# Optimization experiments

Hardware: AMD Instinct MI355X
Metric: run time of the kernel (lower is better)

Reference implementation:

```python
import jax, jax.numpy as jnp
import numpy as np

WH, WW = 12, 12
N_TOK = WH * WW          # 144
DIM = 512
HEADS = 16
NW = 64                  # windows per image
B_ = 256                 # num_windows * batch
CPB_HIDDEN = 512


def _rel_tables():
    # continuous relative coords table (SwinV2 cpb input), shape (1, 2Wh-1, 2Ww-1, 2)
    ch = np.arange(-(WH - 1), WH, dtype=np.float32)
    cw = np.arange(-(WW - 1), WW, dtype=np.float32)
    gh, gw = np.meshgrid(ch, cw, indexing='ij')
    table = np.stack([gh, gw], axis=-1)[None]
    table[..., 0] /= (WH - 1)
    table[..., 1] /= (WW - 1)
    table *= 8.0
    table = np.sign(table) * np.log2(np.abs(table) + 1.0) / np.log2(8.0)
    # relative position index, shape (N, N), values in [0, (2Wh-1)*(2Ww-1))
    coords = np.stack(np.meshgrid(np.arange(WH), np.arange(WW), indexing='ij'))
    cf = coords.reshape(2, -1)
    rel = (cf[:, :, None] - cf[:, None, :]).transpose(1, 2, 0).astype(np.int64)
    rel[..., 0] += WH - 1
    rel[..., 1] += WW - 1
    rel[..., 0] *= 2 * WW - 1
    idx = rel.sum(-1)
    return table.astype(np.float32), idx


def setup_inputs() -> dict:
    key = jax.random.key(0)
    ks = jax.random.split(key, 10)
    table, idx = _rel_tables()
    x = jax.random.normal(ks[0], (B_, N_TOK, DIM), dtype=jnp.float32)
    # 0 / -100 additive mask (shifted-window style), shape (nW, N, N)
    mask = jnp.where(jax.random.uniform(ks[1], (NW, N_TOK, N_TOK)) < 0.9, 0.0, -100.0).astype(jnp.float32)
    s = 0.02
    return {
        'x': x,
        'mask': mask,
        'qkv_w': s * jax.random.normal(ks[2], (3 * DIM, DIM), dtype=jnp.float32),
        'qkv_b': jnp.zeros((3 * DIM,), dtype=jnp.float32),
        'proj_w': s * jax.random.normal(ks[3], (DIM, DIM), dtype=jnp.float32),
        'proj_b': jnp.zeros((DIM,), dtype=jnp.float32),
        'cpb_w1': s * jax.random.normal(ks[4], (CPB_HIDDEN, 2), dtype=jnp.float32),
        'cpb_b1': jnp.zeros((CPB_HIDDEN,), dtype=jnp.float32),
        'cpb_w2': s * jax.random.normal(ks[5], (HEADS, CPB_HIDDEN), dtype=jnp.float32),
        'rel_table': jnp.asarray(table),
        'rel_index': jnp.asarray(idx, dtype=jnp.int32),
    }


def reference(x, mask, qkv_w, qkv_b, proj_w, proj_b, cpb_w1, cpb_b1, cpb_w2, rel_table, rel_index):
    Bw, N, C = x.shape
    H = cpb_w2.shape[0]
    hd = C // H
    scale = hd ** -0.5
    qkv = (x @ qkv_w.T + qkv_b).reshape(Bw, N, 3, H, hd).transpose(2, 0, 3, 1, 4)
    q, k, v = qkv[0], qkv[1], qkv[2]          # each (Bw, H, N, hd)
    attn = jnp.einsum('bhnd,bhmd->bhnm', q * scale, k)
    # continuous relative position bias: MLP on coord table then gather
    tbl = jax.nn.relu(rel_table @ cpb_w1.T + cpb_b1) @ cpb_w2.T   # (1, 2Wh-1, 2Ww-1, H)
    tbl = tbl.reshape(-1, H)
    bias = tbl[rel_index.reshape(-1)].reshape(N, N, H).transpose(2, 0, 1)  # (H, N, N)
    attn = attn + bias[None]
    nW = mask.shape[0]
    attn = attn.reshape(Bw // nW, nW, H, N, N) + mask[None, :, None]
    attn = jax.nn.softmax(attn.reshape(Bw, H, N, N), axis=-1)
    out = jnp.einsum('bhnm,bhmd->bhnd', attn, v).transpose(0, 2, 1, 3).reshape(Bw, N, C)
    return out @ proj_w.T + proj_b
```

## Files before the change

kernel.cpp:

```cpp
#include <hip/hip_runtime.h>


using f32x4  = __attribute__((ext_vector_type(4))) float;
using bf16x8 = __attribute__((ext_vector_type(8))) short;

__device__ __forceinline__ unsigned short f2bf(float f) {
  unsigned u = __float_as_uint(f);
  u = (u + 0x7fffu + ((u >> 16) & 1u)) >> 16;
  return (unsigned short)u;
}
__device__ __forceinline__ float bf2f(unsigned short s) {
  return __uint_as_float(((unsigned)s) << 16);
}

typedef __attribute__((address_space(1))) unsigned int as1_u32;
typedef __attribute__((address_space(3))) unsigned int as3_u32;

__device__ __forceinline__ void gll16(const void* g, void* l) {
  __builtin_amdgcn_global_load_lds((const as1_u32*)g, (as3_u32*)l, 16, 0, 0);
}

__global__ void cvt_f32_bf16(const float4* __restrict__ in,
                             unsigned short* __restrict__ out, int n4) {
  int i = blockIdx.x * blockDim.x + threadIdx.x;
  int stride = gridDim.x * blockDim.x;
  for (; i < n4; i += stride) {
    float4 v = in[i];
    ushort4 o;
    o.x = f2bf(v.x); o.y = f2bf(v.y); o.z = f2bf(v.z); o.w = f2bf(v.w);
    *(ushort4*)(out + (size_t)i * 4) = o;
  }
}

__global__ void cpb_mlp(const float* __restrict__ tbl_in,
                        const float* __restrict__ w1,
                        const float* __restrict__ b1,
                        const float* __restrict__ w2,
                        float* __restrict__ tbl_out) {
  __shared__ float hid[512];
  const int p = blockIdx.x;
  const int t = threadIdx.x;
  float t0 = tbl_in[p * 2 + 0], t1 = tbl_in[p * 2 + 1];
  float hv = fmaf(w1[t * 2 + 0], t0, fmaf(w1[t * 2 + 1], t1, b1[t]));
  hid[t] = fmaxf(hv, 0.f);
  __syncthreads();
  const int head = t >> 5, j = t & 31;
  float partial = 0.f;
  for (int i = j; i < 512; i += 32) partial += hid[i] * w2[head * 512 + i];
#pragma unroll
  for (int mk = 16; mk >= 1; mk >>= 1) partial += __shfl_xor(partial, mk, 32);
  if (j == 0) tbl_out[p * 16 + head] = partial;
}

__global__ void bias_gather(const float* __restrict__ tbl,
                            const int* __restrict__ idx,
                            float* __restrict__ bias_full) {
  int f = blockIdx.x * 256 + threadIdx.x;
  if (f >= 16 * 20736) return;
  int h = f / 20736;
  int p = f - h * 20736;
  bias_full[f] = tbl[idx[p] * 16 + h];
}

template <bool OUT_BF16>
__global__ __launch_bounds__(256) void gemm_bt_k(
    const unsigned short* __restrict__ A, const unsigned short* __restrict__ B,
    const float* __restrict__ bias, void* __restrict__ C, int N, int K) {
  __shared__ __align__(16) unsigned short As[128 * 32];
  __shared__ __align__(16) unsigned short Bs[128 * 32];
  const int tid = threadIdx.x;
  const int wave = tid >> 6, lane = tid & 63;
  const int m0 = blockIdx.y << 7, n0 = blockIdx.x << 7;
  const int wr = wave >> 1, wc = wave & 1;
  const int l15 = lane & 15, l4 = lane >> 4;

  f32x4 acc[4][4] = {};

  const unsigned short* gA = A + (size_t)(m0 + wave * 32 + (lane >> 2)) * K + (lane & 3) * 8;
  const unsigned short* gB = B + (size_t)(n0 + wave * 32 + (lane >> 2)) * K + (lane & 3) * 8;
  unsigned short* lA = As + wave * 32 * 32;
  unsigned short* lB = Bs + wave * 32 * 32;

  for (int k0 = 0; k0 < K; k0 += 32) {
    __syncthreads();
    gll16(gA + k0, lA);
    gll16(gA + k0 + (size_t)16 * K, lA + 16 * 32);
    gll16(gB + k0, lB);
    gll16(gB + k0 + (size_t)16 * K, lB + 16 * 32);
    __syncthreads();
    bf16x8 af[4], bfr[4];
#pragma unroll
    for (int t = 0; t < 4; ++t) {
      af[t]  = *(const bf16x8*)(As + (wr * 64 + t * 16 + l15) * 32 + l4 * 8);
      bfr[t] = *(const bf16x8*)(Bs + (wc * 64 + t * 16 + l15) * 32 + l4 * 8);
    }
#pragma unroll
    for (int i = 0; i < 4; ++i)
#pragma unroll
      for (int j = 0; j < 4; ++j)
        acc[i][j] = __builtin_amdgcn_mfma_f32_16x16x32_bf16(af[i], bfr[j], acc[i][j], 0, 0, 0);
  }

#pragma unroll
  for (int i = 0; i < 4; ++i) {
    int rowb = m0 + wr * 64 + i * 16 + l4 * 4;
#pragma unroll
    for (int j = 0; j < 4; ++j) {
      int col = n0 + wc * 64 + j * 16 + l15;
      float bv = bias[col];
#pragma unroll
      for (int r = 0; r < 4; ++r) {
        size_t off = (size_t)(rowb + r) * N + col;
        float v = acc[i][j][r] + bv;
        if (OUT_BF16) ((unsigned short*)C)[off] = f2bf(v);
        else          ((float*)C)[off] = v;
      }
    }
  }
}

__global__ __launch_bounds__(256) void attn_k(
    const unsigned short* __restrict__ qkv, const float* __restrict__ mask,
    const float* __restrict__ biasf, unsigned short* __restrict__ aout) {
  extern __shared__ __align__(16) char smem[];
  unsigned short* Qs = (unsigned short*)smem;
  unsigned short* Ks = (unsigned short*)(smem + 11520);
  unsigned short* SP = (unsigned short*)(smem + 23040);
  unsigned short* Vt = (unsigned short*)smem;

  const int h = blockIdx.x, b = blockIdx.y;
  const int tid = threadIdx.x;
  const int wave = tid >> 6, lane = tid & 63;
  const int l15 = lane & 15, l4 = lane >> 4;
  const size_t base = (size_t)b * 144 * 1536;

  for (int c = tid; c < 1152; c += 256) {
    int which = (c >= 576) ? 1 : 0;
    int cc = which ? (c - 576) : c;
    int n = cc >> 2, part = cc & 3;
    uint4 v = *(const uint4*)(qkv + base + (size_t)n * 1536 + which * 512 + h * 32 + part * 8);
    unsigned short* dst = (which ? Ks : Qs) + n * 40 + part * 8;
    *(uint4*)dst = v;
  }
  __syncthreads();

  for (int tt = wave; tt < 81; tt += 4) {
    int ti = tt / 9, tj = tt - ti * 9;
    bf16x8 aq = *(const bf16x8*)(Qs + (ti * 16 + l15) * 40 + l4 * 8);
    bf16x8 bk = *(const bf16x8*)(Ks + (tj * 16 + l15) * 40 + l4 * 8);
    f32x4 c = {0.f, 0.f, 0.f, 0.f};
    c = __builtin_amdgcn_mfma_f32_16x16x32_bf16(aq, bk, c, 0, 0, 0);
    unsigned short* scol = SP + tj * 16 + l15;
#pragma unroll
    for (int r = 0; r < 4; ++r)
      scol[(ti * 16 + l4 * 4 + r) * 168] = f2bf(c[r]);
  }
  __syncthreads();

  for (int e = tid; e < 4608; e += 256) {
    int n = e >> 5, d = e & 31;
    Vt[d * 168 + n] = qkv[base + (size_t)n * 1536 + 1024 + h * 32 + d];
  }
  for (int e = tid; e < 768; e += 256) {
    int d = e / 24, n = 144 + (e - (e / 24) * 24);
    Vt[d * 168 + n] = 0;
  }

  {
    const int g = tid >> 4, j = tid & 15;
    const float* mrow = mask + (size_t)(b & 63) * 20736;
    const float* brow = biasf + (size_t)h * 20736;
    const float sc = 0.17677669529663688f;
#pragma unroll
    for (int rr = 0; rr < 9; ++rr) {
      int r = g + rr * 16;
      float lv[9];
      float mx = -3.0e38f;
#pragma unroll
      for (int c2 = 0; c2 < 9; ++c2) {
        int m = j + c2 * 16;
        float s = bf2f(SP[r * 168 + m]);
        float l = fmaf(s, sc, mrow[r * 144 + m] + brow[r * 144 + m]);
        lv[c2] = l;
        mx = fmaxf(mx, l);
      }
#pragma unroll
      for (int mk = 8; mk >= 1; mk >>= 1) mx = fmaxf(mx, __shfl_xor(mx, mk, 16));
      float sum = 0.f;
#pragma unroll
      for (int c2 = 0; c2 < 9; ++c2) {
        lv[c2] = __expf(lv[c2] - mx);
        sum += lv[c2];
      }
#pragma unroll
      for (int mk = 8; mk >= 1; mk >>= 1) sum += __shfl_xor(sum, mk, 16);
      float inv = 1.f / sum;
#pragma unroll
      for (int c2 = 0; c2 < 9; ++c2)
        SP[r * 168 + j + c2 * 16] = f2bf(lv[c2] * inv);
      SP[r * 168 + 144 + j] = 0;
    }
  }
  __syncthreads();

  for (int tt = wave; tt < 18; tt += 4) {
    int ti = tt >> 1, dj = tt & 1;
    f32x4 c = {0.f, 0.f, 0.f, 0.f};
    const unsigned short* pa = SP + (ti * 16 + l15) * 168;
    const unsigned short* vb = Vt + (dj * 16 + l15) * 168;
#pragma unroll
    for (int ks = 0; ks < 5; ++ks) {
      bf16x8 ap = *(const bf16x8*)(pa + ks * 32 + l4 * 8);
      bf16x8 bv = *(const bf16x8*)(vb + ks * 32 + l4 * 8);
      c = __builtin_amdgcn_mfma_f32_16x16x32_bf16(ap, bv, c, 0, 0, 0);
    }
#pragma unroll
    for (int r = 0; r < 4; ++r) {
      int n = ti * 16 + l4 * 4 + r;
      int d = dj * 16 + l15;
      aout[((size_t)(b * 144 + n)) * 512 + h * 32 + d] = f2bf(c[r]);
    }
  }
}

extern "C" void kernel_launch(void* const* d_in, const int* in_sizes, int n_in,
                              void* d_out, int out_size, void* d_ws, size_t ws_size,
                              hipStream_t stream) {
  const float* x        = (const float*)d_in[0];
  const float* mask     = (const float*)d_in[1];
  const float* qkv_w    = (const float*)d_in[2];
  const float* qkv_b    = (const float*)d_in[3];
  const float* proj_w   = (const float*)d_in[4];
  const float* proj_b   = (const float*)d_in[5];
  const float* cpb_w1   = (const float*)d_in[6];
  const float* cpb_b1   = (const float*)d_in[7];
  const float* cpb_w2   = (const float*)d_in[8];
  const float* rel_tab  = (const float*)d_in[9];
  const int*   rel_idx  = (const int*)d_in[10];
  float* out = (float*)d_out;

  char* ws = (char*)d_ws;
  unsigned short* x_bf    = (unsigned short*)(ws);
  unsigned short* wq_bf   = (unsigned short*)(ws + 37748736);
  unsigned short* wp_bf   = (unsigned short*)(ws + 39321600);
  unsigned short* qkv_ws  = (unsigned short*)(ws + 39845888);
  unsigned short* attn_ws = (unsigned short*)(ws + 153092096);
  float*          tbl_ws  = (float*)(ws + 190840832);
  float*          bias_ws = (float*)(ws + 190874688);

  cvt_f32_bf16<<<2048, 256, 0, stream>>>((const float4*)x, x_bf, 4718592);
  cvt_f32_bf16<<<768, 256, 0, stream>>>((const float4*)qkv_w, wq_bf, 196608);
  cvt_f32_bf16<<<256, 256, 0, stream>>>((const float4*)proj_w, wp_bf, 65536);

  cpb_mlp<<<529, 512, 0, stream>>>(rel_tab, cpb_w1, cpb_b1, cpb_w2, tbl_ws);
  bias_gather<<<1296, 256, 0, stream>>>(tbl_ws, rel_idx, bias_ws);

  gemm_bt_k<true><<<dim3(12, 288), 256, 0, stream>>>(x_bf, wq_bf, qkv_b,
                                                     (void*)qkv_ws, 1536, 512);

  hipFuncSetAttribute((const void*)attn_k,
                      hipFuncAttributeMaxDynamicSharedMemorySize, 71424);
  attn_k<<<dim3(16, 256), 256, 71424, stream>>>(qkv_ws, mask, bias_ws, attn_ws);

  gemm_bt_k<false><<<dim3(4, 288), 256, 0, stream>>>(attn_ws, wp_bf, proj_b,
                                                     (void*)out, 512, 512);
}
```

Measured before the change: 425.4 us.

## Fold scale into QKV GEMM, bf16 mask/bias, preload into MFMA accumulator, shrink LDS

```diff
diff --git a/kernel.cpp b/kernel.cpp
--- a/kernel.cpp
+++ b/kernel.cpp
@@ -54,15 +54,15 @@
 
 __global__ void bias_gather(const float* __restrict__ tbl,
                             const int* __restrict__ idx,
-                            float* __restrict__ bias_full) {
+                            unsigned short* __restrict__ bias_bf) {
   int f = blockIdx.x * 256 + threadIdx.x;
   if (f >= 16 * 20736) return;
   int h = f / 20736;
   int p = f - h * 20736;
-  bias_full[f] = tbl[idx[p] * 16 + h];
-}
-
-template <bool OUT_BF16>
+  bias_bf[f] = f2bf(tbl[idx[p] * 16 + h]);
+}
+
+template <bool OUT_BF16, bool QSCALE>
 __global__ __launch_bounds__(256) void gemm_bt_k(
     const unsigned short* __restrict__ A, const unsigned short* __restrict__ B,
     const float* __restrict__ bias, void* __restrict__ C, int N, int K) {
@@ -112,6 +112,7 @@
       for (int r = 0; r < 4; ++r) {
         size_t off = (size_t)(rowb + r) * N + col;
         float v = acc[i][j][r] + bv;
+        if (QSCALE && col < 512) v *= 0.17677669529663688f;
         if (OUT_BF16) ((unsigned short*)C)[off] = f2bf(v);
         else          ((float*)C)[off] = v;
       }
@@ -120,13 +121,12 @@
 }
 
 __global__ __launch_bounds__(256) void attn_k(
-    const unsigned short* __restrict__ qkv, const float* __restrict__ mask,
-    const float* __restrict__ biasf, unsigned short* __restrict__ aout) {
-  extern __shared__ __align__(16) char smem[];
-  unsigned short* Qs = (unsigned short*)smem;
-  unsigned short* Ks = (unsigned short*)(smem + 11520);
-  unsigned short* SP = (unsigned short*)(smem + 23040);
-  unsigned short* Vt = (unsigned short*)smem;
+    const unsigned short* __restrict__ qkv,
+    const unsigned short* __restrict__ maskbf,
+    const unsigned short* __restrict__ biasbf,
+    unsigned short* __restrict__ aout) {
+  __shared__ __align__(16) unsigned short SP[144 * 152];
+  __shared__ __align__(16) unsigned short Vt[32 * 152];
 
   const int h = blockIdx.x, b = blockIdx.y;
   const int tid = threadIdx.x;
@@ -134,43 +134,36 @@
   const int l15 = lane & 15, l4 = lane >> 4;
   const size_t base = (size_t)b * 144 * 1536;
 
-  for (int c = tid; c < 1152; c += 256) {
-    int which = (c >= 576) ? 1 : 0;
-    int cc = which ? (c - 576) : c;
-    int n = cc >> 2, part = cc & 3;
-    uint4 v = *(const uint4*)(qkv + base + (size_t)n * 1536 + which * 512 + h * 32 + part * 8);
-    unsigned short* dst = (which ? Ks : Qs) + n * 40 + part * 8;
-    *(uint4*)dst = v;
-  }
-  __syncthreads();
-
+  for (int c = tid; c < 576; c += 256) {
+    int n = c >> 2, p = c & 3;
+    uint4 v = *(const uint4*)(qkv + base + (size_t)n * 1536 + 1024 + h * 32 + p * 8);
+    unsigned short tmp[8];
+    *(uint4*)tmp = v;
+#pragma unroll
+    for (int j = 0; j < 8; ++j) Vt[(p * 8 + j) * 152 + n] = tmp[j];
+  }
+
+  const unsigned short* mrow = maskbf + (size_t)(b & 63) * 20736;
+  const unsigned short* brow = biasbf + (size_t)h * 20736;
   for (int tt = wave; tt < 81; tt += 4) {
     int ti = tt / 9, tj = tt - ti * 9;
-    bf16x8 aq = *(const bf16x8*)(Qs + (ti * 16 + l15) * 40 + l4 * 8);
-    bf16x8 bk = *(const bf16x8*)(Ks + (tj * 16 + l15) * 40 + l4 * 8);
-    f32x4 c = {0.f, 0.f, 0.f, 0.f};
+    bf16x8 aq = *(const bf16x8*)(qkv + base + (size_t)(ti * 16 + l15) * 1536 + h * 32 + l4 * 8);
+    bf16x8 bk = *(const bf16x8*)(qkv + base + (size_t)(tj * 16 + l15) * 1536 + 512 + h * 32 + l4 * 8);
+    f32x4 c;
+#pragma unroll
+    for (int r = 0; r < 4; ++r) {
+      int rr = ti * 16 + l4 * 4 + r, cc = tj * 16 + l15;
+      c[r] = bf2f(mrow[rr * 144 + cc]) + bf2f(brow[rr * 144 + cc]);
+    }
     c = __builtin_amdgcn_mfma_f32_16x16x32_bf16(aq, bk, c, 0, 0, 0);
-    unsigned short* scol = SP + tj * 16 + l15;
 #pragma unroll
     for (int r = 0; r < 4; ++r)
-      scol[(ti * 16 + l4 * 4 + r) * 168] = f2bf(c[r]);
+      SP[(ti * 16 + l4 * 4 + r) * 152 + tj * 16 + l15] = f2bf(c[r]);
   }
   __syncthreads();
-
-  for (int e = tid; e < 4608; e += 256) {
-    int n = e >> 5, d = e & 31;
-    Vt[d * 168 + n] = qkv[base + (size_t)n * 1536 + 1024 + h * 32 + d];
-  }
-  for (int e = tid; e < 768; e += 256) {
-    int d = e / 24, n = 144 + (e - (e / 24) * 24);
-    Vt[d * 168 + n] = 0;
-  }
 
   {
     const int g = tid >> 4, j = tid & 15;
-    const float* mrow = mask + (size_t)(b & 63) * 20736;
-    const float* brow = biasf + (size_t)h * 20736;
-    const float sc = 0.17677669529663688f;
 #pragma unroll
     for (int rr = 0; rr < 9; ++rr) {
       int r = g + rr * 16;
@@ -178,11 +171,8 @@
       float mx = -3.0e38f;
 #pragma unroll
       for (int c2 = 0; c2 < 9; ++c2) {
-        int m = j + c2 * 16;
-        float s = bf2f(SP[r * 168 + m]);
-        float l = fmaf(s, sc, mrow[r * 144 + m] + brow[r * 144 + m]);
-        lv[c2] = l;
-        mx = fmaxf(mx, l);
+        lv[c2] = bf2f(SP[r * 152 + j + c2 * 16]);
+        mx = fmaxf(mx, lv[c2]);
       }
 #pragma unroll
       for (int mk = 8; mk >= 1; mk >>= 1) mx = fmaxf(mx, __shfl_xor(mx, mk, 16));
@@ -197,8 +187,7 @@
       float inv = 1.f / sum;
 #pragma unroll
       for (int c2 = 0; c2 < 9; ++c2)
-        SP[r * 168 + j + c2 * 16] = f2bf(lv[c2] * inv);
-      SP[r * 168 + 144 + j] = 0;
+        SP[r * 152 + j + c2 * 16] = f2bf(lv[c2] * inv);
     }
   }
   __syncthreads();
@@ -206,12 +195,20 @@
   for (int tt = wave; tt < 18; tt += 4) {
     int ti = tt >> 1, dj = tt & 1;
     f32x4 c = {0.f, 0.f, 0.f, 0.f};
-    const unsigned short* pa = SP + (ti * 16 + l15) * 168;
-    const unsigned short* vb = Vt + (dj * 16 + l15) * 168;
-#pragma unroll
-    for (int ks = 0; ks < 5; ++ks) {
+    const unsigned short* pa = SP + (ti * 16 + l15) * 152;
+    const unsigned short* vb = Vt + (dj * 16 + l15) * 152;
+#pragma unroll
+    for (int ks = 0; ks < 4; ++ks) {
       bf16x8 ap = *(const bf16x8*)(pa + ks * 32 + l4 * 8);
       bf16x8 bv = *(const bf16x8*)(vb + ks * 32 + l4 * 8);
+      c = __builtin_amdgcn_mfma_f32_16x16x32_bf16(ap, bv, c, 0, 0, 0);
+    }
+    {
+      bf16x8 ap = {}, bv = {};
+      if (l4 < 2) {
+        ap = *(const bf16x8*)(pa + 128 + l4 * 8);
+        bv = *(const bf16x8*)(vb + 128 + l4 * 8);
+      }
       c = __builtin_amdgcn_mfma_f32_16x16x32_bf16(ap, bv, c, 0, 0, 0);
     }
 #pragma unroll
@@ -246,22 +243,22 @@
   unsigned short* qkv_ws  = (unsigned short*)(ws + 39845888);
   unsigned short* attn_ws = (unsigned short*)(ws + 153092096);
   float*          tbl_ws  = (float*)(ws + 190840832);
-  float*          bias_ws = (float*)(ws + 190874688);
+  unsigned short* maskbf  = (unsigned short*)(ws + 190874688);
+  unsigned short* biasbf  = (unsigned short*)(ws + 193528896);
 
   cvt_f32_bf16<<<2048, 256, 0, stream>>>((const float4*)x, x_bf, 4718592);
   cvt_f32_bf16<<<768, 256, 0, stream>>>((const float4*)qkv_w, wq_bf, 196608);
   cvt_f32_bf16<<<256, 256, 0, stream>>>((const float4*)proj_w, wp_bf, 65536);
+  cvt_f32_bf16<<<1296, 256, 0, stream>>>((const float4*)mask, maskbf, 331776);
 
   cpb_mlp<<<529, 512, 0, stream>>>(rel_tab, cpb_w1, cpb_b1, cpb_w2, tbl_ws);
-  bias_gather<<<1296, 256, 0, stream>>>(tbl_ws, rel_idx, bias_ws);
-
-  gemm_bt_k<true><<<dim3(12, 288), 256, 0, stream>>>(x_bf, wq_bf, qkv_b,
-                                                     (void*)qkv_ws, 1536, 512);
-
-  hipFuncSetAttribute((const void*)attn_k,
-                      hipFuncAttributeMaxDynamicSharedMemorySize, 71424);
-  attn_k<<<dim3(16, 256), 256, 71424, stream>>>(qkv_ws, mask, bias_ws, attn_ws);
-
-  gemm_bt_k<false><<<dim3(4, 288), 256, 0, stream>>>(attn_ws, wp_bf, proj_b,
-                                                     (void*)out, 512, 512);
-}
+  bias_gather<<<1296, 256, 0, stream>>>(tbl_ws, rel_idx, biasbf);
+
+  gemm_bt_k<true, true><<<dim3(12, 288), 256, 0, stream>>>(
+      x_bf, wq_bf, qkv_b, (void*)qkv_ws, 1536, 512);
+
+  attn_k<<<dim3(16, 256), 256, 0, stream>>>(qkv_ws, maskbf, biasbf, attn_ws);
+
+  gemm_bt_k<false, false><<<dim3(4, 288), 256, 0, stream>>>(
+      attn_ws, wp_bf, proj_b, (void*)out, 512, 512);
+}
```

Result: slower. 434.0 us (+2.0%).
